# Optimization experiments

Hardware: AMD Instinct MI355X
Metric: run time of the kernel (lower is better)

## Reference

```python
import jax, jax.numpy as jnp
import numpy as np

EPS = 1e-8


def setup_inputs() -> dict:
    key = jax.random.key(0)
    k1, k2, k3, k4 = jax.random.split(key, 4)
    B, D, K, L = 131072, 256, 1024, 526
    points = jax.random.normal(k1, (B, D), dtype=jnp.float32)
    labels = jax.random.uniform(k2, (B, L), dtype=jnp.float32)
    centroids = jax.random.normal(k3, (K, D), dtype=jnp.float32)
    running_labels = jax.random.uniform(k4, (K, L), dtype=jnp.float32)
    return {"points": points, "labels": labels, "centroids": centroids,
            "running_labels": running_labels}


def reference(points, labels, centroids, running_labels):
    # One kmeans step: assign -> compute_distance -> compute_distance_labels -> update
    K = centroids.shape[0]
    B = points.shape[0]
    # compute_similarity: squared euclidean distance (B, K), fused matmul form
    x2 = jnp.sum(points * points, axis=-1, keepdims=True)          # (B, 1)
    c2 = jnp.sum(centroids * centroids, axis=-1)                   # (K,)
    d = x2 - 2.0 * (points @ centroids.T) + c2                     # (B, K)
    assignment = jnp.argmin(d, axis=1)                             # (B,)

    # compute_distance: squared dist to assigned centroid + per-cluster dispersion
    sel = centroids[assignment]                                    # (B, D) gather
    dist = jnp.sum(jnp.square(sel - points), axis=-1)              # (B,)
    dispersion = jax.ops.segment_sum(dist, assignment, num_segments=K)

    # compute_distance_labels: cosine distance to assigned cluster label profile
    cl = running_labels[assignment]                                # (B, L) gather
    norm = jnp.sqrt(jnp.sum(jnp.square(labels), axis=-1))
    norm1 = jnp.sqrt(jnp.sum(jnp.square(cl), axis=-1))
    dist_labels = 1.0 - jnp.sum(cl * labels, axis=-1) / (norm * norm1 + EPS)
    dispersion_labels = jax.ops.segment_sum(dist_labels, assignment, num_segments=K)

    # update: scatter segment-sum running statistics
    new_sum = jax.ops.segment_sum(points, assignment, num_segments=K)   # (K, D)
    new_n = jax.ops.segment_sum(jnp.ones((B,), points.dtype), assignment, num_segments=K)
    new_labels = jax.ops.segment_sum(labels, assignment, num_segments=K)  # (K, L)

    return (assignment, dist, dispersion, dist_labels, dispersion_labels,
            new_sum, new_n, new_labels)
```

## Files before the change

### kernel.cpp

```cpp
#include <hip/hip_runtime.h>
#include <float.h>
#include <math.h>

constexpr int Bn = 131072;
constexpr int Dn = 256;
constexpr int Kn = 1024;
constexpr int Ln = 526;
constexpr float EPSF = 1e-8f;

constexpr int CHUNK = 128;
constexpr int MAXCHUNKS = Bn / CHUNK + Kn;

constexpr int BM  = 128;
constexpr int BN  = 128;
constexpr int KC  = 32;
constexpr int NT  = Kn / BN;
constexpr int KCH = Dn / KC;
constexpr int NCH = NT * KCH;

typedef _Float16 f16x8 __attribute__((ext_vector_type(8)));
typedef _Float16 f16x4 __attribute__((ext_vector_type(4)));
typedef float    f32x4 __attribute__((ext_vector_type(4)));

union SMemU {
    _Float16 tiles[2][2][BM][64];
    struct { float t[BM][2]; int k[BM][2]; } red;
};

__device__ __forceinline__ void dma16(const void* g, void* l) {
    __builtin_amdgcn_global_load_lds(
        (const __attribute__((address_space(1))) unsigned int*)g,
        (__attribute__((address_space(3))) unsigned int*)l, 16, 0, 0);
}

__global__ __launch_bounds__(256) void prep_kernel(
    const float* __restrict__ centroids, const float* __restrict__ rlabels,
    float* __restrict__ c2, float* __restrict__ rln, _Float16* __restrict__ cpk)
{
    const int k = blockIdx.x;
    const int t = threadIdx.x;
    float v = centroids[k * Dn + t];
    {
        const int c = t >> 5, j = t & 31;
        const _Float16 h = (_Float16)v;
        const _Float16 l = (_Float16)(v - (float)h);
        cpk[((size_t)k * KCH + c) * 64 + j]      = h;
        cpk[((size_t)k * KCH + c) * 64 + 32 + j] = l;
    }
    float s1 = v * v;
    float s2 = 0.f;
    for (int i = t; i < Ln; i += 256) {
        float u = rlabels[(size_t)k * Ln + i];
        s2 += u * u;
    }
    for (int off = 32; off > 0; off >>= 1) {
        s1 += __shfl_down(s1, off, 64);
        s2 += __shfl_down(s2, off, 64);
    }
    __shared__ float red[8];
    const int wv = t >> 6;
    if ((t & 63) == 0) { red[wv * 2] = s1; red[wv * 2 + 1] = s2; }
    __syncthreads();
    if (t == 0) {
        c2[k]  = red[0] + red[2] + red[4] + red[6];
        rln[k] = sqrtf(red[1] + red[3] + red[5] + red[7]);
    }
}

__global__ __launch_bounds__(256, 2) void assign_kernel(
    const float* __restrict__ points, const _Float16* __restrict__ cpk,
    const float* __restrict__ c2,
    float* __restrict__ o_assign, int* __restrict__ ws_assign,
    float* __restrict__ ws_tmin, int* __restrict__ counts)
{
    __shared__ __align__(16) SMemU sm;
    const int tid  = threadIdx.x;
    const int lane = tid & 63;
    const int wid  = tid >> 6;
    const int wrow = wid >> 1;
    const int wcol = wid & 1;
    const int ln15 = lane & 15;
    const int g    = lane >> 4;
    const int bm0  = blockIdx.x * BM;

    const int arow  = tid >> 1;
    const int ahalf = tid & 1;
    const int r7a   = arow & 7;
    const int s0a   = ahalf * 2;

    const int rowl = lane >> 3;
    const int q8   = lane & 7;

    f32x4 acc[4][4];
#pragma unroll
    for (int i = 0; i < 4; ++i)
#pragma unroll
        for (int j = 0; j < 4; ++j)
#pragma unroll
            for (int r = 0; r < 4; ++r) acc[i][j][r] = 0.f;

    float mint[16];
    int   mink[16];
#pragma unroll
    for (int s = 0; s < 16; ++s) { mint[s] = FLT_MAX; mink[s] = 0; }

    float4 pa[4];
    auto loadA = [&](int t) {
        const int kc = t & 7;
        const float* ap = points + (size_t)(bm0 + arow) * Dn + kc * KC + ahalf * 16;
        pa[0] = *(const float4*)(ap);
        pa[1] = *(const float4*)(ap + 4);
        pa[2] = *(const float4*)(ap + 8);
        pa[3] = *(const float4*)(ap + 12);
    };
    auto dmaB = [&](int t, int buf) {
        const int nt = t >> 3, kc = t & 7;
#pragma unroll
        for (int jj = 0; jj < 4; ++jj) {
            const int p  = wid * 4 + jj;
            const int br = p * 8 + rowl;
            const int srcslot = q8 ^ (br & 7);
            const _Float16* gp = cpk
                + ((size_t)(nt * BN + br) * KCH + kc) * 64 + srcslot * 8;
            dma16(gp, &sm.tiles[buf][1][p * 8][0]);
        }
    };
    auto writeA = [&](int buf) {
        _Float16* Ar = &sm.tiles[buf][0][arow][0];
        const float vs[16] = {pa[0].x, pa[0].y, pa[0].z, pa[0].w,
                              pa[1].x, pa[1].y, pa[1].z, pa[1].w,
                              pa[2].x, pa[2].y, pa[2].z, pa[2].w,
                              pa[3].x, pa[3].y, pa[3].z, pa[3].w};
        f16x8 h0, h1, l0, l1;
#pragma unroll
        for (int u = 0; u < 8; ++u) {
            h0[u] = (_Float16)vs[u];     l0[u] = (_Float16)(vs[u]     - (float)h0[u]);
            h1[u] = (_Float16)vs[8 + u]; l1[u] = (_Float16)(vs[8 + u] - (float)h1[u]);
        }
        *(f16x8*)&Ar[((s0a    ) ^ r7a) * 8] = h0;
        *(f16x8*)&Ar[((s0a + 1) ^ r7a) * 8] = h1;
        *(f16x8*)&Ar[((s0a + 4) ^ r7a) * 8] = l0;
        *(f16x8*)&Ar[((s0a + 5) ^ r7a) * 8] = l1;
    };

    loadA(0);
    dmaB(0, 0);
    writeA(0);
    __syncthreads();

    for (int t = 0; t < NCH; ++t) {
        const int buf = t & 1;
        const bool more = (t + 1) < NCH;
        if (more) { loadA(t + 1); dmaB(t + 1, buf ^ 1); }

        f16x8 ah[4], al[4], bh[4], bl[4];
#pragma unroll
        for (int mi = 0; mi < 4; ++mi) {
            const int r  = wrow * 64 + mi * 16 + ln15;
            const int r7 = r & 7;
            const _Float16* Ar = &sm.tiles[buf][0][r][0];
            ah[mi] = *(const f16x8*)&Ar[((g    ) ^ r7) * 8];
            al[mi] = *(const f16x8*)&Ar[((g + 4) ^ r7) * 8];
        }
#pragma unroll
        for (int nj = 0; nj < 4; ++nj) {
            const int r  = wcol * 64 + nj * 16 + ln15;
            const int r7 = r & 7;
            const _Float16* Br = &sm.tiles[buf][1][r][0];
            bh[nj] = *(const f16x8*)&Br[((g    ) ^ r7) * 8];
            bl[nj] = *(const f16x8*)&Br[((g + 4) ^ r7) * 8];
        }
#pragma unroll
        for (int mi = 0; mi < 4; ++mi)
#pragma unroll
            for (int nj = 0; nj < 4; ++nj) {
                acc[mi][nj] = __builtin_amdgcn_mfma_f32_16x16x32_f16(
                    al[mi], bh[nj], acc[mi][nj], 0, 0, 0);
                acc[mi][nj] = __builtin_amdgcn_mfma_f32_16x16x32_f16(
                    ah[mi], bl[nj], acc[mi][nj], 0, 0, 0);
                acc[mi][nj] = __builtin_amdgcn_mfma_f32_16x16x32_f16(
                    ah[mi], bh[nj], acc[mi][nj], 0, 0, 0);
            }

        if ((t & 7) == 7) {
            const int nt = t >> 3;
            const int nb = nt * BN + wcol * 64 + ln15;
#pragma unroll
            for (int nj = 0; nj < 4; ++nj) {
                const int n = nb + nj * 16;
                const float c2n = c2[n];
#pragma unroll
                for (int mi = 0; mi < 4; ++mi)
#pragma unroll
                    for (int r = 0; r < 4; ++r) {
                        const float tv = fmaf(-2.f, acc[mi][nj][r], c2n);
                        const int s = mi * 4 + r;
                        if (tv < mint[s] || (tv == mint[s] && n < mink[s])) {
                            mint[s] = tv; mink[s] = n;
                        }
                        acc[mi][nj][r] = 0.f;
                    }
            }
        }

        if (more) {
            writeA(buf ^ 1);
            __syncthreads();
        }
    }

#pragma unroll
    for (int s = 0; s < 16; ++s) {
        float tv = mint[s]; int kv = mink[s];
#pragma unroll
        for (int off = 1; off < 16; off <<= 1) {
            const float to = __shfl_xor(tv, off, 64);
            const int   ko = __shfl_xor(kv, off, 64);
            if (to < tv || (to == tv && ko < kv)) { tv = to; kv = ko; }
        }
        mint[s] = tv; mink[s] = kv;
    }
    __syncthreads();
    if (ln15 == 0) {
#pragma unroll
        for (int s = 0; s < 16; ++s) {
            const int pr = wrow * 64 + (s >> 2) * 16 + g * 4 + (s & 3);
            sm.red.t[pr][wcol] = mint[s];
            sm.red.k[pr][wcol] = mink[s];
        }
    }
    __syncthreads();
    if (tid < BM) {
        float bt = sm.red.t[tid][0];
        int   bk = sm.red.k[tid][0];
        const float t1 = sm.red.t[tid][1];
        const int   k1 = sm.red.k[tid][1];
        if (t1 < bt || (t1 == bt && k1 < bk)) { bt = t1; bk = k1; }
        o_assign[bm0 + tid]  = (float)bk;
        ws_assign[bm0 + tid] = bk;
        ws_tmin[bm0 + tid]   = bt;
        atomicAdd(&counts[bk], 1);
    }
}

__global__ __launch_bounds__(1024) void scan_kernel(
    const int* __restrict__ counts, int* __restrict__ offsets,
    int* __restrict__ cursor, float* __restrict__ o_nn,
    int* __restrict__ chunk_off)
{
    __shared__ int s[Kn];
    const int t = threadIdx.x;
    const int c = counts[t];
    o_nn[t] = (float)c;
    s[t] = c;
    __syncthreads();
    for (int off = 1; off < Kn; off <<= 1) {
        const int u = (t >= off) ? s[t - off] : 0;
        __syncthreads();
        s[t] += u;
        __syncthreads();
    }
    const int excl = s[t] - c;
    offsets[t] = excl;
    cursor[t]  = excl;

    const int cc = (c + CHUNK - 1) / CHUNK;
    __syncthreads();
    s[t] = cc;
    __syncthreads();
    for (int off = 1; off < Kn; off <<= 1) {
        const int u = (t >= off) ? s[t - off] : 0;
        __syncthreads();
        s[t] += u;
        __syncthreads();
    }
    chunk_off[t] = s[t] - cc;
    if (t == Kn - 1) chunk_off[Kn] = s[t];
}

__global__ __launch_bounds__(256) void scatter_kernel(
    const int* __restrict__ assigni, int* __restrict__ cursor,
    int* __restrict__ bucket)
{
    const int p = blockIdx.x * 256 + threadIdx.x;
    const int a = assigni[p];
    const int idx = atomicAdd(&cursor[a], 1);
    bucket[idx] = p;
}

__global__ __launch_bounds__(256) void fused_cluster_kernel(
    const float* __restrict__ points, const float* __restrict__ labels,
    const float* __restrict__ rlabels,
    const int* __restrict__ bucket, const int* __restrict__ offsets,
    const int* __restrict__ counts, const int* __restrict__ chunk_off,
    const float* __restrict__ tmin, const float* __restrict__ rln,
    float* __restrict__ o_dist, float* __restrict__ o_disp,
    float* __restrict__ o_dlab, float* __restrict__ o_displab,
    float* __restrict__ o_nsum, float* __restrict__ o_nlab)
{
    const int b = blockIdx.x;
    if (b >= chunk_off[Kn]) return;

    int lo = 0, hi = Kn;
    while (hi - lo > 1) {
        const int mid = (lo + hi) >> 1;
        if (chunk_off[mid] <= b) lo = mid; else hi = mid;
    }
    const int k   = lo;
    const int j   = b - chunk_off[k];
    const int nk  = counts[k];
    const int beg = offsets[k] + j * CHUNK;
    const int nm  = min(nk - j * CHUNK, CHUNK);
    const bool single = (nk <= CHUNK);

    const int tid  = threadIdx.x;
    const int lane = tid & 63;
    const int w    = tid >> 6;

    __shared__ int   sidx[CHUNK];
    __shared__ __align__(16) float srl[528];
    __shared__ float sacc[784];
    __shared__ float sdisp[4], sdlab[4];

    for (int i = tid; i < nm; i += 256) sidx[i] = bucket[beg + i];
    for (int i = tid; i < Ln; i += 256) srl[i] = rlabels[(size_t)k * Ln + i];
    for (int i = tid; i < 784; i += 256) sacc[i] = 0.f;
    __syncthreads();

    const float2 rl0 = *(const float2*)&srl[2 * lane];
    const float2 rl1 = *(const float2*)&srl[2 * (64 + lane)];
    const float2 rl2 = *(const float2*)&srl[2 * (128 + lane)];
    const float2 rl3 = *(const float2*)&srl[2 * (192 + lane)];
    float2 rlT = make_float2(0.f, 0.f);
    if (lane < 7) rlT = *(const float2*)&srl[2 * (256 + lane)];
    const float rlnk = rln[k];

    float4 accP  = make_float4(0.f, 0.f, 0.f, 0.f);
    float2 accL0 = make_float2(0.f, 0.f), accL1 = accL0,
           accL2 = accL0, accL3 = accL0, accLT = accL0;
    float dispacc = 0.f, displabacc = 0.f;

    auto loadM = [&](int i, float4& pv, float2& a, float2& bb, float2& cc,
                     float2& dd, float2& ee, int& pid, float& tm) {
        pid = sidx[i];
        pv = ((const float4*)(points + (size_t)pid * Dn))[lane];
        const float2* l2p = (const float2*)(labels + (size_t)pid * Ln);
        a  = l2p[lane];
        bb = l2p[64 + lane];
        cc = l2p[128 + lane];
        dd = l2p[192 + lane];
        ee = (lane < 7) ? l2p[256 + lane] : make_float2(0.f, 0.f);
        tm = (lane == 0) ? tmin[pid] : 0.f;
    };

    float4 pv0 = make_float4(0,0,0,0), pv1 = pv0, pvX = pv0;
    float2 z2 = make_float2(0.f, 0.f);
    float2 a0 = z2, b0_ = z2, c0 = z2, d0 = z2, e0 = z2;
    float2 a1 = z2, b1_ = z2, c1 = z2, d1 = z2, e1 = z2;
    float2 aX = z2, bX_ = z2, cX = z2, dX = z2, eX = z2;
    int p0 = 0, p1 = 0, pX = 0; float t0 = 0.f, t1 = 0.f, tX = 0.f;

    int i = w;
    if (i < nm)     loadM(i,     pv0, a0, b0_, c0, d0, e0, p0, t0);
    if (i + 4 < nm) loadM(i + 4, pv1, a1, b1_, c1, d1, e1, p1, t1);
    while (i < nm) {
        if (i + 8 < nm) loadM(i + 8, pvX, aX, bX_, cX, dX, eX, pX, tX);

        accP.x += pv0.x; accP.y += pv0.y; accP.z += pv0.z; accP.w += pv0.w;
        accL0.x += a0.x;  accL0.y += a0.y;
        accL1.x += b0_.x; accL1.y += b0_.y;
        accL2.x += c0.x;  accL2.y += c0.y;
        accL3.x += d0.x;  accL3.y += d0.y;
        accLT.x += e0.x;  accLT.y += e0.y;

        float x2m = pv0.x * pv0.x + pv0.y * pv0.y + pv0.z * pv0.z + pv0.w * pv0.w;
        float l2m = a0.x * a0.x + a0.y * a0.y + b0_.x * b0_.x + b0_.y * b0_.y
                  + c0.x * c0.x + c0.y * c0.y + d0.x * d0.x + d0.y * d0.y
                  + e0.x * e0.x + e0.y * e0.y;
        float dtm = a0.x * rl0.x + a0.y * rl0.y + b0_.x * rl1.x + b0_.y * rl1.y
                  + c0.x * rl2.x + c0.y * rl2.y + d0.x * rl3.x + d0.y * rl3.y
                  + e0.x * rlT.x + e0.y * rlT.y;
#pragma unroll
        for (int off = 1; off < 64; off <<= 1) {
            x2m += __shfl_xor(x2m, off, 64);
            l2m += __shfl_xor(l2m, off, 64);
            dtm += __shfl_xor(dtm, off, 64);
        }
        if (lane == 0) {
            const float dist = x2m + t0;
            o_dist[p0] = dist;
            const float dl = 1.0f - dtm / (sqrtf(l2m) * rlnk + EPSF);
            o_dlab[p0] = dl;
            dispacc += dist;
            displabacc += dl;
        }

        pv0 = pv1; a0 = a1; b0_ = b1_; c0 = c1; d0 = d1; e0 = e1; p0 = p1; t0 = t1;
        pv1 = pvX; a1 = aX; b1_ = bX_; c1 = cX; d1 = dX; e1 = eX; p1 = pX; t1 = tX;
        i += 4;
    }

    if (lane == 0) { sdisp[w] = dispacc; sdlab[w] = displabacc; }

    {
        atomicAdd(&sacc[4 * lane + 0], accP.x);
        atomicAdd(&sacc[4 * lane + 1], accP.y);
        atomicAdd(&sacc[4 * lane + 2], accP.z);
        atomicAdd(&sacc[4 * lane + 3], accP.w);
        float* sl = sacc + 256;
        atomicAdd(&sl[2 * lane],           accL0.x); atomicAdd(&sl[2 * lane + 1],       accL0.y);
        atomicAdd(&sl[128 + 2 * lane],     accL1.x); atomicAdd(&sl[128 + 2 * lane + 1], accL1.y);
        atomicAdd(&sl[256 + 2 * lane],     accL2.x); atomicAdd(&sl[256 + 2 * lane + 1], accL2.y);
        atomicAdd(&sl[384 + 2 * lane],     accL3.x); atomicAdd(&sl[384 + 2 * lane + 1], accL3.y);
        if (lane < 7) {
            atomicAdd(&sl[512 + 2 * lane],     accLT.x);
            atomicAdd(&sl[512 + 2 * lane + 1], accLT.y);
        }
    }
    __syncthreads();

    float* np = o_nsum + (size_t)k * Dn;
    float* nl = o_nlab + (size_t)k * Ln;
    const float vP  = sacc[tid];
    const float vL0 = sacc[256 + tid];
    const float vL1 = sacc[512 + tid];
    if (single) {
        np[tid]       = vP;
        nl[tid]       = vL0;
        nl[tid + 256] = vL1;
        if (tid < 14) nl[tid + 512] = sacc[768 + tid];
    } else {
        atomicAdd(&np[tid], vP);
        atomicAdd(&nl[tid], vL0);
        atomicAdd(&nl[tid + 256], vL1);
        if (tid < 14) atomicAdd(&nl[tid + 512], sacc[768 + tid]);
    }
    if (tid == 0) {
        const float dsum  = sdisp[0] + sdisp[1] + sdisp[2] + sdisp[3];
        const float dlsum = sdlab[0] + sdlab[1] + sdlab[2] + sdlab[3];
        if (single) { o_disp[k] = dsum; o_displab[k] = dlsum; }
        else { atomicAdd(&o_disp[k], dsum); atomicAdd(&o_displab[k], dlsum); }
    }
}

extern "C" void kernel_launch(void* const* d_in, const int* in_sizes, int n_in,
                              void* d_out, int out_size, void* d_ws, size_t ws_size,
                              hipStream_t stream)
{
    const float* points    = (const float*)d_in[0];
    const float* labels    = (const float*)d_in[1];
    const float* centroids = (const float*)d_in[2];
    const float* rlabels   = (const float*)d_in[3];

    float* out = (float*)d_out;
    float* o_assign  = out;
    float* o_dist    = out + Bn;
    float* o_disp    = out + 2 * Bn;
    float* o_dlab    = o_disp + Kn;
    float* o_displab = o_dlab + Bn;
    float* o_nsum    = o_displab + Kn;
    float* o_nn      = o_nsum + Kn * Dn;
    float* o_nlab    = o_nn + Kn;

    float* ws        = (float*)d_ws;
    float* c2        = ws;
    float* rln       = ws + Kn;
    float* tmin      = ws + 2 * Kn;
    int*   assigni   = (int*)(ws + 2 * Kn + Bn);
    int*   counts    = assigni + Bn;
    int*   offsets   = counts + Kn;
    int*   cursor    = offsets + Kn;
    int*   bucket    = cursor + Kn;
    int*   chunk_off = bucket + Bn;
    _Float16* cpk    = (_Float16*)(ws + 400000);

    hipMemsetAsync(counts, 0, Kn * sizeof(int), stream);
    hipMemsetAsync(o_disp, 0, Kn * sizeof(float), stream);
    hipMemsetAsync(o_displab, 0, Kn * sizeof(float), stream);
    hipMemsetAsync(o_nsum, 0, (size_t)Kn * Dn * sizeof(float), stream);
    hipMemsetAsync(o_nlab, 0, (size_t)Kn * Ln * sizeof(float), stream);

    prep_kernel<<<Kn, 256, 0, stream>>>(centroids, rlabels, c2, rln, cpk);
    assign_kernel<<<Bn / BM, 256, 0, stream>>>(points, cpk, c2,
                                               o_assign, assigni, tmin, counts);
    scan_kernel<<<1, Kn, 0, stream>>>(counts, offsets, cursor, o_nn, chunk_off);
    scatter_kernel<<<Bn / 256, 256, 0, stream>>>(assigni, cursor, bucket);
    fused_cluster_kernel<<<MAXCHUNKS, 256, 0, stream>>>(
        points, labels, rlabels, bucket, offsets, counts, chunk_off,
        tmin, rln, o_dist, o_disp, o_dlab, o_displab, o_nsum, o_nlab);
}
```

Measured before the change: 796.6 us.

## Enlarge assign GEMM tiles to 256x256 with 8 waves and ping-pong MFMA schedule

The assignment GEMM moves from 128x128 tiles with 4 waves to 256x256 tiles with 8 waves. The main loop is split into four quadrant phases with explicit barriers, setprio around MFMA bursts, and manual vmcnt waits so global loads and LDS writes overlap compute. The argmin indices are packed as 16-bit pairs to save registers. Separately, the scan kernel becomes a wave-shuffle scan, and three small memsets are folded into the prep kernel. Larger tiles cut redundant centroid and point traffic per output, at the cost of register pressure, LDS footprint, and correctness risk in the hand-tuned waitcnt scheduling.

```diff
diff --git a/kernel.cpp b/kernel.cpp
--- a/kernel.cpp
+++ b/kernel.cpp
@@ -11,21 +11,15 @@
 constexpr int CHUNK = 128;
 constexpr int MAXCHUNKS = Bn / CHUNK + Kn;
 
-constexpr int BM  = 128;
-constexpr int BN  = 128;
+constexpr int BM  = 256;
+constexpr int BN  = 256;
 constexpr int KC  = 32;
 constexpr int NT  = Kn / BN;
 constexpr int KCH = Dn / KC;
 constexpr int NCH = NT * KCH;
 
 typedef _Float16 f16x8 __attribute__((ext_vector_type(8)));
-typedef _Float16 f16x4 __attribute__((ext_vector_type(4)));
 typedef float    f32x4 __attribute__((ext_vector_type(4)));
-
-union SMemU {
-    _Float16 tiles[2][2][BM][64];
-    struct { float t[BM][2]; int k[BM][2]; } red;
-};
 
 __device__ __forceinline__ void dma16(const void* g, void* l) {
     __builtin_amdgcn_global_load_lds(
@@ -35,7 +29,9 @@
 
 __global__ __launch_bounds__(256) void prep_kernel(
     const float* __restrict__ centroids, const float* __restrict__ rlabels,
-    float* __restrict__ c2, float* __restrict__ rln, _Float16* __restrict__ cpk)
+    float* __restrict__ c2, float* __restrict__ rln, _Float16* __restrict__ cpk,
+    int* __restrict__ counts, float* __restrict__ o_disp,
+    float* __restrict__ o_displab)
 {
     const int k = blockIdx.x;
     const int t = threadIdx.x;
@@ -64,16 +60,20 @@
     if (t == 0) {
         c2[k]  = red[0] + red[2] + red[4] + red[6];
         rln[k] = sqrtf(red[1] + red[3] + red[5] + red[7]);
-    }
-}
-
-__global__ __launch_bounds__(256, 2) void assign_kernel(
+        counts[k] = 0;
+        o_disp[k] = 0.f;
+        o_displab[k] = 0.f;
+    }
+}
+
+__global__ __launch_bounds__(512, 2) void assign_kernel(
     const float* __restrict__ points, const _Float16* __restrict__ cpk,
     const float* __restrict__ c2,
     float* __restrict__ o_assign, int* __restrict__ ws_assign,
     float* __restrict__ ws_tmin, int* __restrict__ counts)
 {
-    __shared__ __align__(16) SMemU sm;
+    __shared__ __align__(16) _Float16 lds[2][2][256][64];
+
     const int tid  = threadIdx.x;
     const int lane = tid & 63;
     const int wid  = tid >> 6;
@@ -86,23 +86,24 @@
     const int arow  = tid >> 1;
     const int ahalf = tid & 1;
     const int r7a   = arow & 7;
-    const int s0a   = ahalf * 2;
 
     const int rowl = lane >> 3;
     const int q8   = lane & 7;
 
-    f32x4 acc[4][4];
+    f32x4 acc[4][8];
 #pragma unroll
     for (int i = 0; i < 4; ++i)
 #pragma unroll
-        for (int j = 0; j < 4; ++j)
+        for (int j = 0; j < 8; ++j)
 #pragma unroll
             for (int r = 0; r < 4; ++r) acc[i][j][r] = 0.f;
 
     float mint[16];
-    int   mink[16];
-#pragma unroll
-    for (int s = 0; s < 16; ++s) { mint[s] = FLT_MAX; mink[s] = 0; }
+    unsigned int minkp[8];
+#pragma unroll
+    for (int s = 0; s < 16; ++s) mint[s] = FLT_MAX;
+#pragma unroll
+    for (int s = 0; s < 8; ++s) minkp[s] = 0u;
 
     float4 pa[4];
     auto loadA = [&](int t) {
@@ -113,7 +114,7 @@
         pa[2] = *(const float4*)(ap + 8);
         pa[3] = *(const float4*)(ap + 12);
     };
-    auto dmaB = [&](int t, int buf) {
+    auto dmaB = [&](int t, int dbuf) {
         const int nt = t >> 3, kc = t & 7;
 #pragma unroll
         for (int jj = 0; jj < 4; ++jj) {
@@ -122,11 +123,11 @@
             const int srcslot = q8 ^ (br & 7);
             const _Float16* gp = cpk
                 + ((size_t)(nt * BN + br) * KCH + kc) * 64 + srcslot * 8;
-            dma16(gp, &sm.tiles[buf][1][p * 8][0]);
-        }
-    };
-    auto writeA = [&](int buf) {
-        _Float16* Ar = &sm.tiles[buf][0][arow][0];
+            dma16(gp, &lds[1][dbuf][p * 8][0]);
+        }
+    };
+    auto writeA = [&](int dbuf) {
+        _Float16* Ar = &lds[0][dbuf][arow][0];
         const float vs[16] = {pa[0].x, pa[0].y, pa[0].z, pa[0].w,
                               pa[1].x, pa[1].y, pa[1].z, pa[1].w,
                               pa[2].x, pa[2].y, pa[2].z, pa[2].w,
@@ -137,104 +138,147 @@
             h0[u] = (_Float16)vs[u];     l0[u] = (_Float16)(vs[u]     - (float)h0[u]);
             h1[u] = (_Float16)vs[8 + u]; l1[u] = (_Float16)(vs[8 + u] - (float)h1[u]);
         }
-        *(f16x8*)&Ar[((s0a    ) ^ r7a) * 8] = h0;
-        *(f16x8*)&Ar[((s0a + 1) ^ r7a) * 8] = h1;
-        *(f16x8*)&Ar[((s0a + 4) ^ r7a) * 8] = l0;
-        *(f16x8*)&Ar[((s0a + 5) ^ r7a) * 8] = l1;
+        const int s0 = ahalf * 2;
+        *(f16x8*)&Ar[((s0    ) ^ r7a) * 8] = h0;
+        *(f16x8*)&Ar[((s0 + 1) ^ r7a) * 8] = h1;
+        *(f16x8*)&Ar[((s0 + 4) ^ r7a) * 8] = l0;
+        *(f16x8*)&Ar[((s0 + 5) ^ r7a) * 8] = l1;
+    };
+
+    f16x8 ah_[2], al_[2], bh_[4], bl_[4];
+    auto rdA = [&](int buf, int mih) {
+#pragma unroll
+        for (int i = 0; i < 2; ++i) {
+            const int r  = wrow * 64 + (mih * 2 + i) * 16 + ln15;
+            const int r7 = r & 7;
+            const _Float16* Ar = &lds[0][buf][r][0];
+            ah_[i] = *(const f16x8*)&Ar[((g    ) ^ r7) * 8];
+            al_[i] = *(const f16x8*)&Ar[((g + 4) ^ r7) * 8];
+        }
+    };
+    auto rdB = [&](int buf, int njh) {
+#pragma unroll
+        for (int j = 0; j < 4; ++j) {
+            const int r  = wcol * 128 + (njh * 4 + j) * 16 + ln15;
+            const int r7 = r & 7;
+            const _Float16* Br = &lds[1][buf][r][0];
+            bh_[j] = *(const f16x8*)&Br[((g    ) ^ r7) * 8];
+            bl_[j] = *(const f16x8*)&Br[((g + 4) ^ r7) * 8];
+        }
+    };
+    auto mfmaQ = [&](int mih, int njh) {
+#pragma unroll
+        for (int i = 0; i < 2; ++i)
+#pragma unroll
+            for (int j = 0; j < 4; ++j) {
+                f32x4& a = acc[mih * 2 + i][njh * 4 + j];
+                a = __builtin_amdgcn_mfma_f32_16x16x32_f16(al_[i], bh_[j], a, 0, 0, 0);
+                a = __builtin_amdgcn_mfma_f32_16x16x32_f16(ah_[i], bl_[j], a, 0, 0, 0);
+                a = __builtin_amdgcn_mfma_f32_16x16x32_f16(ah_[i], bh_[j], a, 0, 0, 0);
+            }
+    };
+    auto fold = [&](int nt) {
+        const int nb = nt * BN + wcol * 128 + ln15;
+#pragma unroll
+        for (int nj = 0; nj < 8; ++nj) {
+            const int n = nb + nj * 16;
+            const float c2n = c2[n];
+#pragma unroll
+            for (int mi = 0; mi < 4; ++mi)
+#pragma unroll
+                for (int r = 0; r < 4; ++r) {
+                    const float tv = fmaf(-2.f, acc[mi][nj][r], c2n);
+                    const int s = mi * 4 + r;
+                    const int idx = s >> 1;
+                    const unsigned cur = (s & 1) ? (minkp[idx] >> 16)
+                                                 : (minkp[idx] & 0xffffu);
+                    if (tv < mint[s] || (tv == mint[s] && (unsigned)n < cur)) {
+                        mint[s] = tv;
+                        minkp[idx] = (s & 1)
+                            ? ((minkp[idx] & 0x0000ffffu) | ((unsigned)n << 16))
+                            : ((minkp[idx] & 0xffff0000u) | (unsigned)n);
+                    }
+                    acc[mi][nj][r] = 0.f;
+                }
+        }
     };
 
     loadA(0);
     dmaB(0, 0);
+    asm volatile("s_waitcnt vmcnt(4)" ::: "memory");
     writeA(0);
-    __syncthreads();
+    loadA(1);
+    asm volatile("s_waitcnt vmcnt(4)" ::: "memory");
+    asm volatile("s_waitcnt lgkmcnt(0)" ::: "memory");
+    __builtin_amdgcn_s_barrier();
 
     for (int t = 0; t < NCH; ++t) {
-        const int buf = t & 1;
-        const bool more = (t + 1) < NCH;
-        if (more) { loadA(t + 1); dmaB(t + 1, buf ^ 1); }
-
-        f16x8 ah[4], al[4], bh[4], bl[4];
-#pragma unroll
-        for (int mi = 0; mi < 4; ++mi) {
-            const int r  = wrow * 64 + mi * 16 + ln15;
-            const int r7 = r & 7;
-            const _Float16* Ar = &sm.tiles[buf][0][r][0];
-            ah[mi] = *(const f16x8*)&Ar[((g    ) ^ r7) * 8];
-            al[mi] = *(const f16x8*)&Ar[((g + 4) ^ r7) * 8];
-        }
-#pragma unroll
-        for (int nj = 0; nj < 4; ++nj) {
-            const int r  = wcol * 64 + nj * 16 + ln15;
-            const int r7 = r & 7;
-            const _Float16* Br = &sm.tiles[buf][1][r][0];
-            bh[nj] = *(const f16x8*)&Br[((g    ) ^ r7) * 8];
-            bl[nj] = *(const f16x8*)&Br[((g + 4) ^ r7) * 8];
-        }
-#pragma unroll
-        for (int mi = 0; mi < 4; ++mi)
-#pragma unroll
-            for (int nj = 0; nj < 4; ++nj) {
-                acc[mi][nj] = __builtin_amdgcn_mfma_f32_16x16x32_f16(
-                    al[mi], bh[nj], acc[mi][nj], 0, 0, 0);
-                acc[mi][nj] = __builtin_amdgcn_mfma_f32_16x16x32_f16(
-                    ah[mi], bl[nj], acc[mi][nj], 0, 0, 0);
-                acc[mi][nj] = __builtin_amdgcn_mfma_f32_16x16x32_f16(
-                    ah[mi], bh[nj], acc[mi][nj], 0, 0, 0);
-            }
-
-        if ((t & 7) == 7) {
-            const int nt = t >> 3;
-            const int nb = nt * BN + wcol * 64 + ln15;
-#pragma unroll
-            for (int nj = 0; nj < 4; ++nj) {
-                const int n = nb + nj * 16;
-                const float c2n = c2[n];
-#pragma unroll
-                for (int mi = 0; mi < 4; ++mi)
-#pragma unroll
-                    for (int r = 0; r < 4; ++r) {
-                        const float tv = fmaf(-2.f, acc[mi][nj][r], c2n);
-                        const int s = mi * 4 + r;
-                        if (tv < mint[s] || (tv == mint[s] && n < mink[s])) {
-                            mint[s] = tv; mink[s] = n;
-                        }
-                        acc[mi][nj][r] = 0.f;
-                    }
-            }
-        }
-
-        if (more) {
-            writeA(buf ^ 1);
-            __syncthreads();
-        }
-    }
-
+        const int buf = t & 1, nxt = buf ^ 1;
+        const bool last = (t == NCH - 1);
+
+        rdB(buf, 0); rdA(buf, 0);
+        __builtin_amdgcn_s_barrier();
+        __builtin_amdgcn_s_setprio(1); mfmaQ(0, 0); __builtin_amdgcn_s_setprio(0);
+        __builtin_amdgcn_s_barrier();
+
+        rdA(buf, 1);
+        if (!last) dmaB(t + 1, nxt);
+        __builtin_amdgcn_s_barrier();
+        __builtin_amdgcn_s_setprio(1); mfmaQ(1, 0); __builtin_amdgcn_s_setprio(0);
+        __builtin_amdgcn_s_barrier();
+
+        rdB(buf, 1); rdA(buf, 0);
+        if (!last) {
+            asm volatile("s_waitcnt vmcnt(4)" ::: "memory");
+            writeA(nxt);
+        }
+        __builtin_amdgcn_s_barrier();
+        __builtin_amdgcn_s_setprio(1); mfmaQ(0, 1); __builtin_amdgcn_s_setprio(0);
+        asm volatile("s_waitcnt lgkmcnt(0)" ::: "memory");
+        __builtin_amdgcn_s_barrier();
+
+        rdA(buf, 1);
+        if (t < NCH - 2) {
+            loadA(t + 2);
+            asm volatile("s_waitcnt vmcnt(4)" ::: "memory");
+        } else if (t == NCH - 2) {
+            asm volatile("s_waitcnt vmcnt(0)" ::: "memory");
+        }
+        __builtin_amdgcn_s_setprio(1); mfmaQ(1, 1); __builtin_amdgcn_s_setprio(0);
+        if ((t & 7) == 7) fold(t >> 3);
+        __builtin_amdgcn_s_barrier();
+    }
+
+    float rt[16]; int rk[16];
 #pragma unroll
     for (int s = 0; s < 16; ++s) {
-        float tv = mint[s]; int kv = mink[s];
+        float tv = mint[s];
+        int kv = (int)((s & 1) ? (minkp[s >> 1] >> 16) : (minkp[s >> 1] & 0xffffu));
 #pragma unroll
         for (int off = 1; off < 16; off <<= 1) {
             const float to = __shfl_xor(tv, off, 64);
             const int   ko = __shfl_xor(kv, off, 64);
             if (to < tv || (to == tv && ko < kv)) { tv = to; kv = ko; }
         }
-        mint[s] = tv; mink[s] = kv;
-    }
-    __syncthreads();
+        rt[s] = tv; rk[s] = kv;
+    }
+    __syncthreads();
+    float* redt = (float*)&lds[0][0][0][0];
+    int*   redk = (int*)(redt + 512);
     if (ln15 == 0) {
 #pragma unroll
         for (int s = 0; s < 16; ++s) {
             const int pr = wrow * 64 + (s >> 2) * 16 + g * 4 + (s & 3);
-            sm.red.t[pr][wcol] = mint[s];
-            sm.red.k[pr][wcol] = mink[s];
+            redt[pr * 2 + wcol] = rt[s];
+            redk[pr * 2 + wcol] = rk[s];
         }
     }
     __syncthreads();
     if (tid < BM) {
-        float bt = sm.red.t[tid][0];
-        int   bk = sm.red.k[tid][0];
-        const float t1 = sm.red.t[tid][1];
-        const int   k1 = sm.red.k[tid][1];
+        float bt = redt[tid * 2];
+        int   bk = redk[tid * 2];
+        const float t1 = redt[tid * 2 + 1];
+        const int   k1 = redk[tid * 2 + 1];
         if (t1 < bt || (t1 == bt && k1 < bk)) { bt = t1; bk = k1; }
         o_assign[bm0 + tid]  = (float)bk;
         ws_assign[bm0 + tid] = bk;
@@ -248,34 +292,60 @@
     int* __restrict__ cursor, float* __restrict__ o_nn,
     int* __restrict__ chunk_off)
 {
-    __shared__ int s[Kn];
+    __shared__ int wsum[16];
+    __shared__ int wbase[16];
     const int t = threadIdx.x;
+    const int lane = t & 63;
+    const int w = t >> 6;
+
     const int c = counts[t];
     o_nn[t] = (float)c;
-    s[t] = c;
-    __syncthreads();
-    for (int off = 1; off < Kn; off <<= 1) {
-        const int u = (t >= off) ? s[t - off] : 0;
-        __syncthreads();
-        s[t] += u;
-        __syncthreads();
-    }
-    const int excl = s[t] - c;
-    offsets[t] = excl;
-    cursor[t]  = excl;
+
+    int v = c;
+#pragma unroll
+    for (int off = 1; off < 64; off <<= 1) {
+        const int u = __shfl_up(v, off, 64);
+        if (lane >= off) v += u;
+    }
+    if (lane == 63) wsum[w] = v;
+    __syncthreads();
+    if (w == 0 && lane < 16) {
+        int s = wsum[lane];
+#pragma unroll
+        for (int off = 1; off < 16; off <<= 1) {
+            const int u = __shfl_up(s, off, 64);
+            if (lane >= off) s += u;
+        }
+        wbase[lane] = s;
+    }
+    __syncthreads();
+    const int incl = ((w == 0) ? 0 : wbase[w - 1]) + v;
+    offsets[t] = incl - c;
+    cursor[t]  = incl - c;
+    __syncthreads();
 
     const int cc = (c + CHUNK - 1) / CHUNK;
-    __syncthreads();
-    s[t] = cc;
-    __syncthreads();
-    for (int off = 1; off < Kn; off <<= 1) {
-        const int u = (t >= off) ? s[t - off] : 0;
-        __syncthreads();
-        s[t] += u;
-        __syncthreads();
-    }
-    chunk_off[t] = s[t] - cc;
-    if (t == Kn - 1) chunk_off[Kn] = s[t];
+    int v2 = cc;
+#pragma unroll
+    for (int off = 1; off < 64; off <<= 1) {
+        const int u = __shfl_up(v2, off, 64);
+        if (lane >= off) v2 += u;
+    }
+    if (lane == 63) wsum[w] = v2;
+    __syncthreads();
+    if (w == 0 && lane < 16) {
+        int s = wsum[lane];
+#pragma unroll
+        for (int off = 1; off < 16; off <<= 1) {
+            const int u = __shfl_up(s, off, 64);
+            if (lane >= off) s += u;
+        }
+        wbase[lane] = s;
+    }
+    __syncthreads();
+    const int incl2 = ((w == 0) ? 0 : wbase[w - 1]) + v2;
+    chunk_off[t] = incl2 - cc;
+    if (t == Kn - 1) chunk_off[Kn] = incl2;
 }
 
 __global__ __launch_bounds__(256) void scatter_kernel(
@@ -474,14 +544,12 @@
     int*   chunk_off = bucket + Bn;
     _Float16* cpk    = (_Float16*)(ws + 400000);
 
-    hipMemsetAsync(counts, 0, Kn * sizeof(int), stream);
-    hipMemsetAsync(o_disp, 0, Kn * sizeof(float), stream);
-    hipMemsetAsync(o_displab, 0, Kn * sizeof(float), stream);
     hipMemsetAsync(o_nsum, 0, (size_t)Kn * Dn * sizeof(float), stream);
     hipMemsetAsync(o_nlab, 0, (size_t)Kn * Ln * sizeof(float), stream);
 
-    prep_kernel<<<Kn, 256, 0, stream>>>(centroids, rlabels, c2, rln, cpk);
-    assign_kernel<<<Bn / BM, 256, 0, stream>>>(points, cpk, c2,
+    prep_kernel<<<Kn, 256, 0, stream>>>(centroids, rlabels, c2, rln, cpk,
+                                        counts, o_disp, o_displab);
+    assign_kernel<<<Bn / BM, 512, 0, stream>>>(points, cpk, c2,
                                                o_assign, assigni, tmin, counts);
     scan_kernel<<<1, Kn, 0, stream>>>(counts, offsets, cursor, o_nn, chunk_off);
     scatter_kernel<<<Bn / 256, 256, 0, stream>>>(assigni, cursor, bucket);
```

Measured after the change: 806.6 us. No clear change (+1.3%).
